# Kernel optimization log

Hardware: AMD Instinct MI355X
Metric: run time of the kernel (lower is better)

Reference implementation:

```python
import jax, jax.numpy as jnp
import numpy as np

STRIDE = 1
PAD = 1
DIL = 1
TEMP = 30.0


def setup_inputs() -> dict:
    key = jax.random.key(0)
    ks = jax.random.split(key, 9)
    B, C, OC, H, W, E, K, HID = 16, 64, 64, 128, 128, 4, 3, 16
    return {
        "x": jax.random.normal(ks[0], (B, C, H, W), dtype=jnp.float32),
        "cw1": jax.random.normal(ks[1], (HID, C), dtype=jnp.float32) * 0.1,   # 1x1 conv C->HID
        "cw2": jax.random.normal(ks[2], (E * OC, HID), dtype=jnp.float32) * 0.1,  # 1x1 conv HID->E*OC
        "w1": jax.random.normal(ks[3], (E, OC, C, K, K), dtype=jnp.float32) * 0.05,
        "w2": jax.random.normal(ks[4], (E, OC, OC, K, K), dtype=jnp.float32) * 0.05,
        "w3": jax.random.normal(ks[5], (E, OC, OC, K, K), dtype=jnp.float32) * 0.05,
        "b1": jax.random.normal(ks[6], (E, OC), dtype=jnp.float32) * 0.05,
        "b2": jax.random.normal(ks[7], (E, OC), dtype=jnp.float32) * 0.05,
        "b3": jax.random.normal(ks[8], (E, OC), dtype=jnp.float32) * 0.05,
    }


def _batched_conv(x, w, b):
    """Per-sample conv: x (B,C,H,W), w (B,OC,C,K,K), b (B,OC).
    Equivalent to torch's groups=B trick on a flattened (1, B*C, H, W) input."""
    def one(xi, wi, bi):
        y = jax.lax.conv_general_dilated(
            xi[None], wi,
            window_strides=(STRIDE, STRIDE),
            padding=[(PAD, PAD), (PAD, PAD)],
            rhs_dilation=(DIL, DIL),
            dimension_numbers=("NCHW", "OIHW", "NCHW"),
        )[0]
        return y + bi[:, None, None]
    return jax.vmap(one)(x, w, b)


def reference(x, cw1, cw2, w1, w2, w3, b1, b2, b3):
    B = x.shape[0]
    E, OC = w1.shape[0], w1.shape[1]
    # ControlModule: global avg pool -> 1x1 conv -> relu -> 1x1 conv -> softmax over experts
    pooled = x.mean(axis=(2, 3))                       # (B, C)
    hid = jax.nn.relu(pooled @ cw1.T)                  # (B, HID)
    logits = (hid @ cw2.T).reshape(B, OC, E)           # (B, OC, E); channel layout (oc e)
    coeff = jax.nn.softmax(logits / TEMP, axis=2)      # (B, OC, E)
    # Per-sample expert-mixed weights/biases (einsum 'bce,ech->bch' in source)
    agg_w = lambda w: jnp.einsum("boe,eoikl->boikl", coeff, w)
    agg_b = lambda b: jnp.einsum("boe,eo->bo", coeff, b)
    out = _batched_conv(x, agg_w(w1), agg_b(b1))
    out = _batched_conv(out, agg_w(w2), agg_b(b2))
    out = _batched_conv(out, agg_w(w3), agg_b(b3))
    return out
```

## Files before the change

### kernel.cpp

```cpp
#include <hip/hip_runtime.h>
#include <math.h>

#define B_   16
#define C_   64
#define OC_  64
#define H_   128
#define W_   128
#define E_   4
#define HID_ 16
#define HW_  (H_ * W_)
#define TEMP_ 30.0f

#define PSTR ((size_t)B_ * HW_ * 32)

typedef float f32x4 __attribute__((ext_vector_type(4)));
typedef short s16x8 __attribute__((ext_vector_type(8)));
typedef short s16x4 __attribute__((ext_vector_type(4)));

__device__ __forceinline__ unsigned short f2bf(float f) {
    unsigned u = __float_as_uint(f);
    u = u + 0x7FFFu + ((u >> 16) & 1u);
    return (unsigned short)(u >> 16);
}
__device__ __forceinline__ float bf2f(unsigned short h) {
    return __uint_as_float(((unsigned)h) << 16);
}

__global__ void pool_kernel(const float* __restrict__ x, float* __restrict__ pooled) {
    int bc = blockIdx.x;
    const float4* xp = (const float4*)(x + (size_t)bc * HW_);
    float s = 0.f;
    for (int i = threadIdx.x; i < HW_ / 4; i += 256) {
        float4 v = xp[i];
        s += v.x + v.y + v.z + v.w;
    }
    for (int off = 32; off; off >>= 1) s += __shfl_down(s, off, 64);
    __shared__ float red[4];
    int lane = threadIdx.x & 63, wv = threadIdx.x >> 6;
    if (lane == 0) red[wv] = s;
    __syncthreads();
    if (threadIdx.x == 0)
        pooled[bc] = (red[0] + red[1] + red[2] + red[3]) * (1.0f / (float)HW_);
}

__global__ void control_kernel(const float* __restrict__ pooled,
                               const float* __restrict__ cw1,
                               const float* __restrict__ cw2,
                               const float* __restrict__ b1,
                               const float* __restrict__ b2,
                               const float* __restrict__ b3,
                               float* __restrict__ coeff,
                               float* __restrict__ ab_all) {
    int b = blockIdx.x;
    int t = threadIdx.x;
    __shared__ float pl[C_];
    __shared__ float hid[HID_];
    pl[t] = pooled[b * C_ + t];
    __syncthreads();
    if (t < HID_) {
        float a = 0.f;
        for (int c = 0; c < C_; ++c) a = fmaf(pl[c], cw1[t * C_ + c], a);
        hid[t] = fmaxf(a, 0.f);
    }
    __syncthreads();
    float l[E_];
#pragma unroll
    for (int e = 0; e < E_; ++e) {
        float a = 0.f;
#pragma unroll
        for (int h = 0; h < HID_; ++h) a = fmaf(hid[h], cw2[(t * E_ + e) * HID_ + h], a);
        l[e] = a * (1.0f / TEMP_);
    }
    float m = fmaxf(fmaxf(l[0], l[1]), fmaxf(l[2], l[3]));
    float p[E_], s = 0.f;
#pragma unroll
    for (int e = 0; e < E_; ++e) { p[e] = expf(l[e] - m); s += p[e]; }
    float inv = 1.0f / s;
#pragma unroll
    for (int e = 0; e < E_; ++e) { p[e] *= inv; coeff[(b * OC_ + t) * E_ + e] = p[e]; }
    float a1 = 0.f, a2 = 0.f, a3 = 0.f;
#pragma unroll
    for (int e = 0; e < E_; ++e) {
        a1 = fmaf(p[e], b1[e * OC_ + t], a1);
        a2 = fmaf(p[e], b2[e * OC_ + t], a2);
        a3 = fmaf(p[e], b3[e * OC_ + t], a3);
    }
    ab_all[0 * B_ * OC_ + b * OC_ + t] = a1;
    ab_all[1 * B_ * OC_ + b * OC_ + t] = a2;
    ab_all[2 * B_ * OC_ + b * OC_ + t] = a3;
}

__global__ void aggw_split(const float* __restrict__ coeff,
                           const float* __restrict__ w1,
                           const float* __restrict__ w2,
                           const float* __restrict__ w3,
                           unsigned short* __restrict__ Wh1, unsigned short* __restrict__ Wl1,
                           unsigned short* __restrict__ Wh2, unsigned short* __restrict__ Wl2,
                           unsigned short* __restrict__ Wh3, unsigned short* __restrict__ Wl3) {
    int layer = blockIdx.y;
    const float* w = (layer == 0) ? w1 : (layer == 1) ? w2 : w3;
    unsigned short* Wh = (layer == 0) ? Wh1 : (layer == 1) ? Wh2 : Wh3;
    unsigned short* Wl = (layer == 0) ? Wl1 : (layer == 1) ? Wl2 : Wl3;

    int idx = blockIdx.x * 256 + threadIdx.x;
    int c   = idx & 63;
    int r   = idx >> 6;
    int tap = r % 9;
    int r2  = r / 9;
    int oc  = r2 & 63;
    int b   = r2 >> 6;

    float s = 0.f;
#pragma unroll
    for (int e = 0; e < E_; ++e)
        s = fmaf(coeff[(b * OC_ + oc) * E_ + e],
                 w[(((size_t)e * OC_ + oc) * C_ + c) * 9 + tap], s);
    unsigned short h = f2bf(s);
    Wh[idx] = h;
    Wl[idx] = f2bf(s - bf2f(h));
}

__global__ void xcvt_kernel(const float* __restrict__ x,
                            unsigned short* __restrict__ Xs) {
    __shared__ float tr[64][65];
    const int b   = blockIdx.y;
    const int hw0 = blockIdx.x * 64;
    const int t   = threadIdx.x;
    const int l   = t & 63;
    const int wv  = t >> 6;
    const float* src = x + (size_t)b * C_ * HW_;
#pragma unroll
    for (int i = 0; i < 16; ++i) {
        int c = wv * 16 + i;
        tr[l][c] = src[(size_t)c * HW_ + hw0 + l];
    }
    __syncthreads();
#pragma unroll
    for (int i = 0; i < 2; ++i) {
        int g  = t + i * 256;
        int px = g >> 3;
        int cg = (g & 7) << 3;
        s16x8 hv, lv;
#pragma unroll
        for (int j = 0; j < 8; ++j) {
            float v = tr[px][cg + j];
            unsigned short h = f2bf(v);
            hv[j] = (short)h;
            lv[j] = (short)f2bf(v - bf2f(h));
        }
        int chunk = cg >> 5;
        int off   = cg & 31;
        size_t base = ((size_t)b * HW_ + hw0 + px) * 32 + off;
        *(s16x8*)(Xs + (size_t)(0 + chunk) * PSTR + base) = hv;
        *(s16x8*)(Xs + (size_t)(2 + chunk) * PSTR + base) = lv;
    }
}

#define NG 4160
__launch_bounds__(512, 1)
__global__ void conv_mfma(const unsigned short* __restrict__ Xs,
                          const unsigned short* __restrict__ Wh,
                          const unsigned short* __restrict__ Wl,
                          const float* __restrict__ bias,
                          unsigned short* __restrict__ Ys,
                          float* __restrict__ Yf,
                          int final_layer) {
    const int bid  = blockIdx.x;
    const int wg   = (bid & 7) * 128 + (bid >> 3);
    const int b    = wg >> 6;
    const int py0  = (wg & 63) * 2;

    const int t  = threadIdx.x;
    const int l  = t & 63;
    const int wv = t >> 6;
    const int lq = l >> 4;
    const int ln = l & 15;
    const int rw = wv & 1;
    const int qx = wv >> 1;

    __shared__ __align__(16) unsigned short ldsA[NG * 8];
    __shared__ __align__(16) unsigned short ldsB[NG * 8];

    f32x4 acc[4][2];
#pragma unroll
    for (int o = 0; o < 4; ++o)
#pragma unroll
        for (int n = 0; n < 2; ++n)
#pragma unroll
            for (int r = 0; r < 4; ++r) acc[o][n][r] = 0.f;

    const size_t pbase = (size_t)b * HW_ * 32;
    const size_t wbase = (size_t)b * OC_ * 9 * 64;

    s16x8 stg[9];

#define ISSUE(ch)                                                              \
    {                                                                          \
        _Pragma("unroll")                                                      \
        for (int i = 0; i < 9; ++i) {                                          \
            if (i < 8 || t < (NG - 4096)) {                                    \
                int g    = t + i * 512;                                        \
                int row  = g / 1040;                                           \
                int rem  = g - row * 1040;                                     \
                int pr   = rem >> 4;                                           \
                int slot = rem & 15;                                           \
                int s_lin = slot ^ (pr & 7);                                   \
                int k = s_lin >> 3, u = (s_lin >> 2) & 1, q = s_lin & 3;       \
                int ir = py0 + row - 1;                                        \
                int ic = 2 * pr + u - 1;                                       \
                s16x8 v;                                                       \
                _Pragma("unroll")                                              \
                for (int j = 0; j < 8; ++j) v[j] = 0;                          \
                if ((unsigned)ir < (unsigned)H_ && (unsigned)ic < (unsigned)W_)\
                    v = *(const s16x8*)(Xs + (size_t)(k * 2 + (ch)) * PSTR + pbase \
                        + ((size_t)(ir * W_ + ic)) * 32 + q * 8);              \
                stg[i] = v;                                                    \
            }                                                                  \
        }                                                                      \
    }

#define WRITE_STG(BUF)                                                         \
    {                                                                          \
        _Pragma("unroll")                                                      \
        for (int i = 0; i < 9; ++i)                                            \
            if (i < 8 || t < (NG - 4096))                                      \
                *(s16x8*)&(BUF)[(t + i * 512) * 8] = stg[i];                   \
    }

#define TAPS(BUF, CBASE)                                                       \
    {                                                                          \
        s16x8 Ah[2][4], Al[2][4];                                              \
        _Pragma("unroll")                                                      \
        for (int oct = 0; oct < 4; ++oct) {                                    \
            size_t woff = wbase + ((size_t)((oct * 16 + ln) * 9)) * 64         \
                          + (CBASE) + lq * 8;                                  \
            Ah[0][oct] = *(const s16x8*)(Wh + woff);                           \
            Al[0][oct] = *(const s16x8*)(Wl + woff);                           \
        }                                                                      \
        _Pragma("unroll")                                                      \
        for (int tap = 0; tap < 9; ++tap) {                                    \
            const int pp = tap & 1;                                            \
            if (tap < 8) {                                                     \
                _Pragma("unroll")                                              \
                for (int oct = 0; oct < 4; ++oct) {                            \
                    size_t woff = wbase + ((size_t)((oct * 16 + ln) * 9 + tap + 1)) * 64 \
                                  + (CBASE) + lq * 8;                          \
                    Ah[pp ^ 1][oct] = *(const s16x8*)(Wh + woff);              \
                    Al[pp ^ 1][oct] = *(const s16x8*)(Wl + woff);              \
                }                                                              \
            }                                                                  \
            const int ky  = tap / 3;                                           \
            const int kx  = tap - ky * 3;                                       \
            const int row = rw + ky;                                           \
            s16x8 Bh[2], Bl[2];                                                \
            _Pragma("unroll")                                                  \
            for (int nt = 0; nt < 2; ++nt) {                                   \
                int col = qx * 32 + nt * 16 + ln + kx;                         \
                int pr  = col >> 1, u = col & 1;                               \
                int bse = (row * 65 + pr) << 4;                                \
                Bh[nt] = *(const s16x8*)&(BUF)[(bse + ((u * 4 + lq) ^ (pr & 7))) << 3];      \
                Bl[nt] = *(const s16x8*)&(BUF)[(bse + ((8 + u * 4 + lq) ^ (pr & 7))) << 3];  \
            }                                                                  \
            _Pragma("unroll")                                                  \
            for (int oct = 0; oct < 4; ++oct)                                  \
                _Pragma("unroll")                                              \
                for (int nt = 0; nt < 2; ++nt)                                 \
                    acc[oct][nt] = __builtin_amdgcn_mfma_f32_16x16x32_bf16(    \
                        Ah[pp][oct], Bh[nt], acc[oct][nt], 0, 0, 0);           \
            _Pragma("unroll")                                                  \
            for (int oct = 0; oct < 4; ++oct)                                  \
                _Pragma("unroll")                                              \
                for (int nt = 0; nt < 2; ++nt)                                 \
                    acc[oct][nt] = __builtin_amdgcn_mfma_f32_16x16x32_bf16(    \
                        Al[pp][oct], Bh[nt], acc[oct][nt], 0, 0, 0);           \
            _Pragma("unroll")                                                  \
            for (int oct = 0; oct < 4; ++oct)                                  \
                _Pragma("unroll")                                              \
                for (int nt = 0; nt < 2; ++nt)                                 \
                    acc[oct][nt] = __builtin_amdgcn_mfma_f32_16x16x32_bf16(    \
                        Ah[pp][oct], Bl[nt], acc[oct][nt], 0, 0, 0);           \
        }                                                                      \
    }

    ISSUE(0);
    WRITE_STG(ldsA);
    ISSUE(1);
    __syncthreads();

    TAPS(ldsA, 0);
    WRITE_STG(ldsB);
    __syncthreads();

    TAPS(ldsB, 32);

    float bia[4][4];
#pragma unroll
    for (int oct = 0; oct < 4; ++oct)
#pragma unroll
        for (int r = 0; r < 4; ++r)
            bia[oct][r] = bias[b * OC_ + oct * 16 + lq * 4 + r];

    const int orow = py0 + rw;
    if (!final_layer) {
#pragma unroll
        for (int oct = 0; oct < 4; ++oct)
#pragma unroll
            for (int nt = 0; nt < 2; ++nt) {
                int px = qx * 32 + nt * 16 + ln;
                size_t pxl = (size_t)b * HW_ + orow * W_ + px;
                int oc0   = oct * 16 + lq * 4;
                int chunk = oc0 >> 5;
                int off   = oc0 & 31;
                s16x4 hv, lv;
#pragma unroll
                for (int r = 0; r < 4; ++r) {
                    float v = acc[oct][nt][r] + bia[oct][r];
                    unsigned short h = f2bf(v);
                    hv[r] = (short)h;
                    lv[r] = (short)f2bf(v - bf2f(h));
                }
                *(s16x4*)(Ys + (size_t)(0 + chunk) * PSTR + pxl * 32 + off) = hv;
                *(s16x4*)(Ys + (size_t)(2 + chunk) * PSTR + pxl * 32 + off) = lv;
            }
    } else {
#pragma unroll
        for (int oct = 0; oct < 4; ++oct)
#pragma unroll
            for (int nt = 0; nt < 2; ++nt) {
                int px = qx * 32 + nt * 16 + ln;
#pragma unroll
                for (int r = 0; r < 4; ++r) {
                    int oc = oct * 16 + lq * 4 + r;
                    Yf[((size_t)(b * OC_ + oc)) * HW_ + orow * W_ + px] =
                        acc[oct][nt][r] + bia[oct][r];
                }
            }
    }
#undef ISSUE
#undef WRITE_STG
#undef TAPS
}

extern "C" void kernel_launch(void* const* d_in, const int* in_sizes, int n_in,
                              void* d_out, int out_size, void* d_ws, size_t ws_size,
                              hipStream_t stream) {
    const float* x   = (const float*)d_in[0];
    const float* cw1 = (const float*)d_in[1];
    const float* cw2 = (const float*)d_in[2];
    const float* w1  = (const float*)d_in[3];
    const float* w2  = (const float*)d_in[4];
    const float* w3  = (const float*)d_in[5];
    const float* b1  = (const float*)d_in[6];
    const float* b2  = (const float*)d_in[7];
    const float* b3  = (const float*)d_in[8];

    char* ws = (char*)d_ws;
    float* pooled = (float*)(ws + 0);
    float* coeff  = (float*)(ws + 4096);
    float* ab_all = (float*)(ws + 20480);
    const size_t WSZ = (size_t)B_ * OC_ * 9 * 64 * 2;
    unsigned short* Wh1 = (unsigned short*)(ws + 32768);
    unsigned short* Wl1 = (unsigned short*)(ws + 32768 + 1 * WSZ);
    unsigned short* Wh2 = (unsigned short*)(ws + 32768 + 2 * WSZ);
    unsigned short* Wl2 = (unsigned short*)(ws + 32768 + 3 * WSZ);
    unsigned short* Wh3 = (unsigned short*)(ws + 32768 + 4 * WSZ);
    unsigned short* Wl3 = (unsigned short*)(ws + 32768 + 5 * WSZ);
    const size_t SOFF = 32768 + 6 * WSZ;
    const size_t SSZ  = 4 * PSTR * 2;
    unsigned short* S0 = (unsigned short*)(ws + SOFF);
    unsigned short* S1 = (unsigned short*)(ws + SOFF + SSZ);

    float* ab1 = ab_all;
    float* ab2 = ab_all + B_ * OC_;
    float* ab3 = ab_all + 2 * B_ * OC_;

    pool_kernel<<<B_ * C_, 256, 0, stream>>>(x, pooled);
    control_kernel<<<B_, 64, 0, stream>>>(pooled, cw1, cw2, b1, b2, b3, coeff, ab_all);
    {
        dim3 g(2304, 3);
        aggw_split<<<g, 256, 0, stream>>>(coeff, w1, w2, w3,
                                          Wh1, Wl1, Wh2, Wl2, Wh3, Wl3);
    }
    {
        dim3 g(HW_ / 64, B_);
        xcvt_kernel<<<g, 256, 0, stream>>>(x, S0);
    }
    conv_mfma<<<1024, 512, 0, stream>>>(S0, Wh1, Wl1, ab1, S1, nullptr, 0);
    conv_mfma<<<1024, 512, 0, stream>>>(S1, Wh2, Wl2, ab2, S0, nullptr, 0);
    conv_mfma<<<1024, 512, 0, stream>>>(S0, Wh3, Wl3, ab3, nullptr, (float*)d_out, 1);
}
```

Before: 618.8 us.

## Use direct global-to-LDS loads with one output row per smaller workgroup

The conv kernel now uses 256-thread workgroups, each computing one output row, with launch bounds allowing three blocks per CU. The register-staged double buffer is replaced by a single LDS tile filled through global_load_lds. Padding and out-of-range lanes read from a zeroed scratch pointer instead of taking a conditional branch. This drops the VGPR staging and LDS write instructions and raises occupancy, but it loses the overlap between loading the second channel chunk and computing the first, adds extra barriers, and each row now reloads a 3-row halo, so more input is read per output.

```diff
diff --git a/kernel.cpp b/kernel.cpp
--- a/kernel.cpp
+++ b/kernel.cpp
@@ -156,30 +156,28 @@
     }
 }
 
-#define NG 4160
-__launch_bounds__(512, 1)
+__launch_bounds__(256, 3)
 __global__ void conv_mfma(const unsigned short* __restrict__ Xs,
                           const unsigned short* __restrict__ Wh,
                           const unsigned short* __restrict__ Wl,
                           const float* __restrict__ bias,
+                          const unsigned short* __restrict__ zp,
                           unsigned short* __restrict__ Ys,
                           float* __restrict__ Yf,
                           int final_layer) {
-    const int bid  = blockIdx.x;
-    const int wg   = (bid & 7) * 128 + (bid >> 3);
-    const int b    = wg >> 6;
-    const int py0  = (wg & 63) * 2;
+    const int bid = blockIdx.x;
+    const int wg  = (bid & 7) * 256 + (bid >> 3);
+    const int b   = wg >> 7;
+    const int py  = wg & 127;
 
     const int t  = threadIdx.x;
     const int l  = t & 63;
     const int wv = t >> 6;
     const int lq = l >> 4;
     const int ln = l & 15;
-    const int rw = wv & 1;
-    const int qx = wv >> 1;
-
-    __shared__ __align__(16) unsigned short ldsA[NG * 8];
-    __shared__ __align__(16) unsigned short ldsB[NG * 8];
+    const int qx = wv;
+
+    __shared__ __align__(16) unsigned short lds_x[3136 * 8];
 
     f32x4 acc[4][2];
 #pragma unroll
@@ -192,42 +190,35 @@
     const size_t pbase = (size_t)b * HW_ * 32;
     const size_t wbase = (size_t)b * OC_ * 9 * 64;
 
-    s16x8 stg[9];
-
-#define ISSUE(ch)                                                              \
+#define ISSUE_LDS(ch)                                                          \
     {                                                                          \
         _Pragma("unroll")                                                      \
-        for (int i = 0; i < 9; ++i) {                                          \
-            if (i < 8 || t < (NG - 4096)) {                                    \
-                int g    = t + i * 512;                                        \
+        for (int i = 0; i < 13; ++i) {                                         \
+            int j = wv + i * 4;                                                \
+            if (j < 49) {                                                      \
+                int g    = j * 64 + l;                                         \
                 int row  = g / 1040;                                           \
                 int rem  = g - row * 1040;                                     \
                 int pr   = rem >> 4;                                           \
                 int slot = rem & 15;                                           \
                 int s_lin = slot ^ (pr & 7);                                   \
                 int k = s_lin >> 3, u = (s_lin >> 2) & 1, q = s_lin & 3;       \
-                int ir = py0 + row - 1;                                        \
+                int ir = py + row - 1;                                         \
                 int ic = 2 * pr + u - 1;                                       \
-                s16x8 v;                                                       \
-                _Pragma("unroll")                                              \
-                for (int j = 0; j < 8; ++j) v[j] = 0;                          \
-                if ((unsigned)ir < (unsigned)H_ && (unsigned)ic < (unsigned)W_)\
-                    v = *(const s16x8*)(Xs + (size_t)(k * 2 + (ch)) * PSTR + pbase \
-                        + ((size_t)(ir * W_ + ic)) * 32 + q * 8);              \
-                stg[i] = v;                                                    \
+                const unsigned short* sp = zp;                                 \
+                if (g < 3120 && (unsigned)ir < (unsigned)H_ &&                 \
+                    (unsigned)ic < (unsigned)W_)                               \
+                    sp = Xs + (size_t)(k * 2 + (ch)) * PSTR + pbase            \
+                         + ((size_t)(ir * W_ + ic)) * 32 + q * 8;              \
+                __builtin_amdgcn_global_load_lds(                              \
+                    (const __attribute__((address_space(1))) unsigned int*)sp, \
+                    (__attribute__((address_space(3))) unsigned int*)&lds_x[(size_t)j * 64 * 8], \
+                    16, 0, 0);                                                 \
             }                                                                  \
         }                                                                      \
     }
 
-#define WRITE_STG(BUF)                                                         \
-    {                                                                          \
-        _Pragma("unroll")                                                      \
-        for (int i = 0; i < 9; ++i)                                            \
-            if (i < 8 || t < (NG - 4096))                                      \
-                *(s16x8*)&(BUF)[(t + i * 512) * 8] = stg[i];                   \
-    }
-
-#define TAPS(BUF, CBASE)                                                       \
+#define TAPS(CBASE)                                                            \
     {                                                                          \
         s16x8 Ah[2][4], Al[2][4];                                              \
         _Pragma("unroll")                                                      \
@@ -249,17 +240,16 @@
                     Al[pp ^ 1][oct] = *(const s16x8*)(Wl + woff);              \
                 }                                                              \
             }                                                                  \
-            const int ky  = tap / 3;                                           \
-            const int kx  = tap - ky * 3;                                       \
-            const int row = rw + ky;                                           \
+            const int ky = tap / 3;                                            \
+            const int kx = tap - ky * 3;                                       \
             s16x8 Bh[2], Bl[2];                                                \
             _Pragma("unroll")                                                  \
             for (int nt = 0; nt < 2; ++nt) {                                   \
                 int col = qx * 32 + nt * 16 + ln + kx;                         \
                 int pr  = col >> 1, u = col & 1;                               \
-                int bse = (row * 65 + pr) << 4;                                \
-                Bh[nt] = *(const s16x8*)&(BUF)[(bse + ((u * 4 + lq) ^ (pr & 7))) << 3];      \
-                Bl[nt] = *(const s16x8*)&(BUF)[(bse + ((8 + u * 4 + lq) ^ (pr & 7))) << 3];  \
+                int bse = (ky * 65 + pr) << 4;                                 \
+                Bh[nt] = *(const s16x8*)&lds_x[(size_t)(bse + ((u * 4 + lq) ^ (pr & 7))) << 3];     \
+                Bl[nt] = *(const s16x8*)&lds_x[(size_t)(bse + ((8 + u * 4 + lq) ^ (pr & 7))) << 3]; \
             }                                                                  \
             _Pragma("unroll")                                                  \
             for (int oct = 0; oct < 4; ++oct)                                  \
@@ -282,16 +272,13 @@
         }                                                                      \
     }
 
-    ISSUE(0);
-    WRITE_STG(ldsA);
-    ISSUE(1);
-    __syncthreads();
-
-    TAPS(ldsA, 0);
-    WRITE_STG(ldsB);
-    __syncthreads();
-
-    TAPS(ldsB, 32);
+    ISSUE_LDS(0);
+    __syncthreads();
+    TAPS(0);
+    __syncthreads();
+    ISSUE_LDS(1);
+    __syncthreads();
+    TAPS(32);
 
     float bia[4][4];
 #pragma unroll
@@ -300,14 +287,13 @@
         for (int r = 0; r < 4; ++r)
             bia[oct][r] = bias[b * OC_ + oct * 16 + lq * 4 + r];
 
-    const int orow = py0 + rw;
     if (!final_layer) {
 #pragma unroll
         for (int oct = 0; oct < 4; ++oct)
 #pragma unroll
             for (int nt = 0; nt < 2; ++nt) {
                 int px = qx * 32 + nt * 16 + ln;
-                size_t pxl = (size_t)b * HW_ + orow * W_ + px;
+                size_t pxl = (size_t)b * HW_ + py * W_ + px;
                 int oc0   = oct * 16 + lq * 4;
                 int chunk = oc0 >> 5;
                 int off   = oc0 & 31;
@@ -331,13 +317,12 @@
 #pragma unroll
                 for (int r = 0; r < 4; ++r) {
                     int oc = oct * 16 + lq * 4 + r;
-                    Yf[((size_t)(b * OC_ + oc)) * HW_ + orow * W_ + px] =
+                    Yf[((size_t)(b * OC_ + oc)) * HW_ + py * W_ + px] =
                         acc[oct][nt][r] + bia[oct][r];
                 }
             }
     }
-#undef ISSUE
-#undef WRITE_STG
+#undef ISSUE_LDS
 #undef TAPS
 }
 
@@ -369,10 +354,13 @@
     const size_t SSZ  = 4 * PSTR * 2;
     unsigned short* S0 = (unsigned short*)(ws + SOFF);
     unsigned short* S1 = (unsigned short*)(ws + SOFF + SSZ);
+    unsigned short* zp = (unsigned short*)(ws + SOFF + 2 * SSZ);
 
     float* ab1 = ab_all;
     float* ab2 = ab_all + B_ * OC_;
     float* ab3 = ab_all + 2 * B_ * OC_;
+
+    hipMemsetAsync(zp, 0, 64, stream);
 
     pool_kernel<<<B_ * C_, 256, 0, stream>>>(x, pooled);
     control_kernel<<<B_, 64, 0, stream>>>(pooled, cw1, cw2, b1, b2, b3, coeff, ab_all);
@@ -385,7 +373,7 @@
         dim3 g(HW_ / 64, B_);
         xcvt_kernel<<<g, 256, 0, stream>>>(x, S0);
     }
-    conv_mfma<<<1024, 512, 0, stream>>>(S0, Wh1, Wl1, ab1, S1, nullptr, 0);
-    conv_mfma<<<1024, 512, 0, stream>>>(S1, Wh2, Wl2, ab2, S0, nullptr, 0);
-    conv_mfma<<<1024, 512, 0, stream>>>(S0, Wh3, Wl3, ab3, nullptr, (float*)d_out, 1);
-}
+    conv_mfma<<<2048, 256, 0, stream>>>(S0, Wh1, Wl1, ab1, zp, S1, nullptr, 0);
+    conv_mfma<<<2048, 256, 0, stream>>>(S1, Wh2, Wl2, ab2, zp, S0, nullptr, 0);
+    conv_mfma<<<2048, 256, 0, stream>>>(S0, Wh3, Wl3, ab3, zp, nullptr, (float*)d_out, 1);
+}
```

Measured after the change: 684.7 us. +10.7%, slower.
